# Performance work log

Hardware: AMD Instinct MI355X
Metric: run time of the kernel (lower is better)

Reference implementation:

```python
import jax, jax.numpy as jnp
import numpy as np

N_HEAD = 16
NEG = -1.0e9


def setup_inputs() -> dict:
    key = jax.random.key(0)
    k1, k2, k3 = jax.random.split(key, 3)
    B, T, C = 4, 2048, 1024
    x = jax.random.normal(k1, (B, T, C), dtype=jnp.float32)
    # torch Linear(C, 3C, bias=False): weight [3C, C], y = x @ W.T
    w_attn = jax.random.normal(k2, (3 * C, C), dtype=jnp.float32) * (1.0 / np.sqrt(C))
    w_proj = jax.random.normal(k3, (C, C), dtype=jnp.float32) * (1.0 / np.sqrt(C))
    return {"x": x, "w_attn": w_attn, "w_proj": w_proj}


def reference(x, w_attn, w_proj):
    B, T, C = x.shape
    hd = C // N_HEAD
    qkv = x @ w_attn.T  # [B,T,3C]
    q, k, v = jnp.split(qkv, 3, axis=2)
    # [B,T,C] -> [B,H,T,hd]
    q = q.reshape(B, T, N_HEAD, hd).transpose(0, 2, 1, 3)
    k = k.reshape(B, T, N_HEAD, hd).transpose(0, 2, 1, 3)
    v = v.reshape(B, T, N_HEAD, hd).transpose(0, 2, 1, 3)
    att = jnp.einsum('bhqd,bhkd->bhqk', q, k) * (1.0 / np.sqrt(hd))
    causal = jnp.tril(jnp.ones((T, T), dtype=bool))
    att = jnp.where(causal[None, None, :, :], att, NEG)
    att = jax.nn.softmax(att, axis=-1)
    y = jnp.einsum('bhqk,bhkd->bhqd', att, v)  # [B,H,T,hd]
    y = y.transpose(0, 2, 1, 3).reshape(B, T, C)
    return y @ w_proj.T
```

## Files before the change

### kernel.cpp

```cpp
#include <hip/hip_runtime.h>
#include <hip/hip_bf16.h>

typedef __bf16 bf16x8_t __attribute__((ext_vector_type(8)));
typedef __bf16 bf16x4_t __attribute__((ext_vector_type(4)));
typedef float f32x4_t __attribute__((ext_vector_type(4)));

__device__ __forceinline__ void gload_lds16(const void* g, void* l) {
    __builtin_amdgcn_global_load_lds((const __attribute__((address_space(1))) void*)g,
                                     (__attribute__((address_space(3))) void*)l, 16, 0, 0);
}

__global__ void f2bf_kernel(const float* __restrict__ in, __bf16* __restrict__ out, int n) {
    int i = (blockIdx.x * blockDim.x + threadIdx.x) * 4;
    if (i >= n) return;
    float4 v = *(const float4*)(in + i);
    bf16x4_t o;
    o[0] = (__bf16)v.x; o[1] = (__bf16)v.y; o[2] = (__bf16)v.z; o[3] = (__bf16)v.w;
    *(bf16x4_t*)(out + i) = o;
}

template <typename OutT>
__global__ __launch_bounds__(256) void gemm_bt(const __bf16* __restrict__ A,
                                               const __bf16* __restrict__ Bt,
                                               OutT* __restrict__ C,
                                               int M, int N, int K) {
    __shared__ __bf16 As[128 * 32];
    __shared__ __bf16 Bs[128 * 32];

    const int tid  = threadIdx.x;
    const int lane = tid & 63;
    const int wid  = tid >> 6;
    const int wm   = wid >> 1;
    const int wn   = wid & 1;

    const int nwg = gridDim.x * gridDim.y;
    int fl = blockIdx.y * gridDim.x + blockIdx.x;
    fl = (fl & 7) * (nwg >> 3) + (fl >> 3);
    const int m0 = (fl / gridDim.x) * 128;
    const int n0 = (fl % gridDim.x) * 128;

    const int lr = lane & 15;
    const int lk = (lane >> 4) * 8;
    const int cr = (lane >> 4) * 4;

    f32x4_t acc[4][4];
    for (int i = 0; i < 4; ++i)
        for (int j = 0; j < 4; ++j)
            acc[i][j] = (f32x4_t){0.f, 0.f, 0.f, 0.f};

    for (int k0 = 0; k0 < K; k0 += 32) {
        __syncthreads();
        for (int i = 0; i < 2; ++i) {
            int flat = i * 256 + tid;
            int row  = flat >> 2;
            int col  = (flat & 3) * 8;
            gload_lds16(&A[(size_t)(m0 + row) * K + k0 + col], &As[(size_t)(i * 256 + wid * 64) * 8]);
            gload_lds16(&Bt[(size_t)(n0 + row) * K + k0 + col], &Bs[(size_t)(i * 256 + wid * 64) * 8]);
        }
        __syncthreads();

        bf16x8_t af[4], bfr[4];
        for (int mf = 0; mf < 4; ++mf)
            af[mf] = *(const bf16x8_t*)&As[(wm * 64 + mf * 16 + lr) * 32 + lk];
        for (int nf = 0; nf < 4; ++nf)
            bfr[nf] = *(const bf16x8_t*)&Bs[(wn * 64 + nf * 16 + lr) * 32 + lk];
        for (int mf = 0; mf < 4; ++mf)
            for (int nf = 0; nf < 4; ++nf)
                acc[mf][nf] = __builtin_amdgcn_mfma_f32_16x16x32_bf16(af[mf], bfr[nf], acc[mf][nf], 0, 0, 0);
    }

    for (int mf = 0; mf < 4; ++mf)
        for (int nf = 0; nf < 4; ++nf)
            for (int r = 0; r < 4; ++r) {
                int row = m0 + wm * 64 + mf * 16 + cr + r;
                int col = n0 + wn * 64 + nf * 16 + lr;
                C[(size_t)row * N + col] = (OutT)acc[mf][nf][r];
            }
}

__global__ __launch_bounds__(512, 4) void attn_kernel(const __bf16* __restrict__ qkv,
                                                      __bf16* __restrict__ y) {
    const int T = 2048, C3 = 3072;
    const int orig = blockIdx.x;
    const int bidx = ((orig & 7) << 6) + (orig >> 3);
    const int pair = bidx & 7;
    const int h    = (bidx >> 3) & 15;
    const int b    = bidx >> 7;

    __shared__ __bf16 Ks[128 * 64];
    __shared__ __bf16 Vt[2][64 * 72];
    __shared__ __bf16 Ps[8 * 16 * 136];

    const int tid  = threadIdx.x;
    const int lane = tid & 63;
    const int w    = tid >> 6;
    const int lr   = lane & 15;
    const int lg   = lane >> 4;
    const int lk   = lg * 8;

    const __bf16* qg = qkv + (size_t)b * T * C3 + h * 64;
    const __bf16* kg = qg + 1024;
    const __bf16* vg = qg + 2048;

    const float CE    = 0.125f * 1.44269504f;
    const float DEFER = 44.0f;

    const int r0    = tid >> 3;
    const int kcol  = (tid & 7) * 8;
    const int kslot = ((tid & 7) ^ (r0 & 7)) << 3;
    const int vks   = r0 ^ ((tid & 7) << 3);

    __bf16* Pw = &Ps[w * 16 * 136];

    for (int pass = 0; pass < 2; ++pass) {
        const int qs  = pass ? 15 - pair : pair;
        const int qt0 = qs * 128;
        const int nt  = qs + 1;

        bf16x8_t qf0, qf1;
        {
            const __bf16* qrow = qg + (size_t)(qt0 + w * 16 + lr) * C3;
            qf0 = *(const bf16x8_t*)&qrow[lk];
            qf1 = *(const bf16x8_t*)&qrow[32 + lk];
        }

        bf16x8_t ka = *(const bf16x8_t*)&kg[(size_t)r0 * C3 + kcol];
        bf16x8_t kb = *(const bf16x8_t*)&kg[(size_t)(64 + r0) * C3 + kcol];
        bf16x8_t va = *(const bf16x8_t*)&vg[(size_t)r0 * C3 + kcol];
        bf16x8_t vb = *(const bf16x8_t*)&vg[(size_t)(64 + r0) * C3 + kcol];

        f32x4_t o_acc[4];
#pragma unroll
        for (int i = 0; i < 4; ++i) o_acc[i] = (f32x4_t){0.f, 0.f, 0.f, 0.f};
        float m_r = -3.0e38f, l_r = 0.f;

        for (int t = 0; t < nt; ++t) {
            __syncthreads();

            *(bf16x8_t*)&Ks[r0 * 64 + kslot] = ka;
            *(bf16x8_t*)&Ks[(64 + r0) * 64 + kslot] = kb;
#pragma unroll
            for (int j = 0; j < 8; ++j) Vt[0][(kcol + j) * 72 + vks] = va[j];
#pragma unroll
            for (int j = 0; j < 8; ++j) Vt[1][(kcol + j) * 72 + vks] = vb[j];

            __syncthreads();

            if (t + 1 < nt) {
                const size_t kb0 = (size_t)(t + 1) * 128;
                ka = *(const bf16x8_t*)&kg[(kb0 + r0) * C3 + kcol];
                kb = *(const bf16x8_t*)&kg[(kb0 + 64 + r0) * C3 + kcol];
                va = *(const bf16x8_t*)&vg[(kb0 + r0) * C3 + kcol];
                vb = *(const bf16x8_t*)&vg[(kb0 + 64 + r0) * C3 + kcol];
            }

            f32x4_t s[8];
#pragma unroll
            for (int c = 0; c < 8; ++c) {
                const int key = c * 16 + lr;
                const int sw  = (key & 7) << 3;
                bf16x8_t kfa = *(const bf16x8_t*)&Ks[key * 64 + (lk ^ sw)];
                bf16x8_t kfb = *(const bf16x8_t*)&Ks[key * 64 + ((32 + lk) ^ sw)];
                s[c] = __builtin_amdgcn_mfma_f32_16x16x32_bf16(kfa, qf0, (f32x4_t){0.f, 0.f, 0.f, 0.f}, 0, 0, 0);
                s[c] = __builtin_amdgcn_mfma_f32_16x16x32_bf16(kfb, qf1, s[c], 0, 0, 0);
            }

            if (t == nt - 1) {
                const int ql = w * 16 + lr;
#pragma unroll
                for (int c = 0; c < 8; ++c)
#pragma unroll
                    for (int r = 0; r < 4; ++r)
                        if (c * 16 + lg * 4 + r > ql) s[c][r] = -1.0e30f;
            }

            float pm = s[0][0];
#pragma unroll
            for (int c = 0; c < 8; ++c)
#pragma unroll
                for (int r = 0; r < 4; ++r) pm = fmaxf(pm, s[c][r]);

            if (!__all(pm <= m_r + DEFER)) {
                pm = fmaxf(pm, __shfl_xor(pm, 16));
                pm = fmaxf(pm, __shfl_xor(pm, 32));
                const float mn    = fmaxf(m_r, pm);
                const float alpha = exp2f((m_r - mn) * CE);
                l_r *= alpha;
#pragma unroll
                for (int dt = 0; dt < 4; ++dt)
#pragma unroll
                    for (int r = 0; r < 4; ++r) o_acc[dt][r] *= alpha;
                m_r = mn;
            }
            const float mce = m_r * CE;

            float rs = 0.f;
#pragma unroll
            for (int c = 0; c < 8; ++c) {
                bf16x4_t pk;
#pragma unroll
                for (int r = 0; r < 4; ++r) {
                    float pv = exp2f(fmaf(s[c][r], CE, -mce));
                    rs += pv;
                    pk[r] = (__bf16)pv;
                }
                *(bf16x4_t*)&Pw[lr * 136 + c * 16 + lg * 4] = pk;
            }
            rs += __shfl_xor(rs, 16);
            rs += __shfl_xor(rs, 32);
            l_r += rs;

#pragma unroll
            for (int hf = 0; hf < 2; ++hf) {
                bf16x8_t pb0 = *(const bf16x8_t*)&Pw[lr * 136 + hf * 64 + lk];
                bf16x8_t pb1 = *(const bf16x8_t*)&Pw[lr * 136 + hf * 64 + 32 + lk];
#pragma unroll
                for (int dt = 0; dt < 4; ++dt) {
                    const int d   = dt * 16 + lr;
                    const int sw2 = ((d >> 3) & 7) << 3;
                    bf16x8_t vb0 = *(const bf16x8_t*)&Vt[hf][d * 72 + (lk ^ sw2)];
                    bf16x8_t vb1 = *(const bf16x8_t*)&Vt[hf][d * 72 + ((32 + lk) ^ sw2)];
                    o_acc[dt] = __builtin_amdgcn_mfma_f32_16x16x32_bf16(vb0, pb0, o_acc[dt], 0, 0, 0);
                    o_acc[dt] = __builtin_amdgcn_mfma_f32_16x16x32_bf16(vb1, pb1, o_acc[dt], 0, 0, 0);
                }
            }
        }

        const float inv = 1.0f / l_r;
        const int q = qt0 + w * 16 + lr;
#pragma unroll
        for (int dt = 0; dt < 4; ++dt) {
            bf16x4_t ov;
#pragma unroll
            for (int r = 0; r < 4; ++r) ov[r] = (__bf16)(o_acc[dt][r] * inv);
            *(bf16x4_t*)&y[(size_t)(b * T + q) * 1024 + h * 64 + dt * 16 + lg * 4] = ov;
        }
    }
}

extern "C" void kernel_launch(void* const* d_in, const int* in_sizes, int n_in,
                              void* d_out, int out_size, void* d_ws, size_t ws_size,
                              hipStream_t stream) {
    const float* x      = (const float*)d_in[0];
    const float* w_attn = (const float*)d_in[1];
    const float* w_proj = (const float*)d_in[2];
    float* out = (float*)d_out;

    char* ws = (char*)d_ws;
    __bf16* xb   = (__bf16*)(ws);
    __bf16* wab  = (__bf16*)(ws + 16777216);
    __bf16* wpb  = (__bf16*)(ws + 23068672);
    __bf16* qkvb = (__bf16*)(ws + 25165824);
    __bf16* yb   = (__bf16*)(ws + 75497472);

    f2bf_kernel<<<8192, 256, 0, stream>>>(x, xb, 8388608);
    f2bf_kernel<<<3072, 256, 0, stream>>>(w_attn, wab, 3145728);
    f2bf_kernel<<<1024, 256, 0, stream>>>(w_proj, wpb, 1048576);

    gemm_bt<__bf16><<<dim3(24, 64), 256, 0, stream>>>(xb, wab, qkvb, 8192, 3072, 1024);

    attn_kernel<<<512, 512, 0, stream>>>(qkvb, yb);

    gemm_bt<float><<<dim3(8, 64), 256, 0, stream>>>(yb, wpb, out, 8192, 1024, 1024);
}
```

Before: 190.9 us.

## Add 512-thread 128x256 double-buffered QKV GEMM with swizzled LDS and setprio

Replaces the QKV projection GEMM with a new kernel that uses 512-thread blocks and 128x256 output tiles with a K-step of 64. Tiles are double-buffered in LDS through direct global-to-LDS loads, with an XOR swizzle to avoid bank conflicts. A vmcnt-based wait lets the next tile's loads overlap the current tile's MFMAs, and s_setprio raises wave priority during the math. The larger tile is meant to improve operand reuse and hide load latency. In exchange it uses more LDS and registers per block, and the grid drops to 768 blocks.

```diff
diff --git a/kernel.cpp b/kernel.cpp
--- a/kernel.cpp
+++ b/kernel.cpp
@@ -17,6 +17,122 @@
     bf16x4_t o;
     o[0] = (__bf16)v.x; o[1] = (__bf16)v.y; o[2] = (__bf16)v.z; o[3] = (__bf16)v.w;
     *(bf16x4_t*)(out + i) = o;
+}
+
+__global__ __launch_bounds__(512, 2) void gemm1_8ph(const __bf16* __restrict__ A,
+                                                    const __bf16* __restrict__ Bt,
+                                                    __bf16* __restrict__ C,
+                                                    int M, int N, int K) {
+    __shared__ __bf16 AsB[2][16 * 512];
+    __shared__ __bf16 BsB[2][32 * 512];
+
+    const int tid  = threadIdx.x;
+    const int lane = tid & 63;
+    const int wid  = tid >> 6;
+    const int wm   = wid >> 2;
+    const int wn   = wid & 3;
+
+    const int nwg   = gridDim.x;
+    const int ntile = N >> 8;
+    int fl = blockIdx.x;
+    fl = (fl & 7) * (nwg >> 3) + (fl >> 3);
+    const int m0 = (fl / ntile) * 128;
+    const int n0 = (fl % ntile) * 256;
+
+    const int lr = lane & 15;
+    const int lg = lane >> 4;
+    const int cr = lg * 4;
+    const int srow = lane >> 3;
+    const int gcol = (((lane & 7) ^ srow) << 3);
+
+    f32x4_t acc[4][4];
+#pragma unroll
+    for (int i = 0; i < 4; ++i)
+#pragma unroll
+        for (int j = 0; j < 4; ++j)
+            acc[i][j] = (f32x4_t){0.f, 0.f, 0.f, 0.f};
+
+    const int NT = K >> 6;
+
+    auto stage = [&](int kt, int buf) {
+        const __bf16* Ab = A + (size_t)m0 * K + kt * 64;
+        const __bf16* Bb = Bt + (size_t)n0 * K + kt * 64;
+        __bf16* Al = &AsB[buf][0];
+        __bf16* Bl = &BsB[buf][0];
+#pragma unroll
+        for (int j = 0; j < 6; ++j) {
+            int seg = wid * 6 + j;
+            if (seg < 16) {
+                gload_lds16(Ab + (size_t)(seg * 8 + srow) * K + gcol, Al + seg * 512);
+            } else {
+                int s2 = seg - 16;
+                gload_lds16(Bb + (size_t)(s2 * 8 + srow) * K + gcol, Bl + s2 * 512);
+            }
+        }
+    };
+
+    stage(0, 0);
+
+    for (int kt = 0; kt < NT; ++kt) {
+        const int cur = kt & 1;
+        const bool pf = (kt + 1 < NT);
+        if (pf) stage(kt + 1, cur ^ 1);
+
+        if (pf) asm volatile("s_waitcnt vmcnt(6)" ::: "memory");
+        else    asm volatile("s_waitcnt vmcnt(0)" ::: "memory");
+        __builtin_amdgcn_sched_barrier(0);
+        __builtin_amdgcn_s_barrier();
+        __builtin_amdgcn_sched_barrier(0);
+
+        const __bf16* Al = &AsB[cur][0];
+        const __bf16* Bl = &BsB[cur][0];
+
+        bf16x8_t af[4][2];
+#pragma unroll
+        for (int mf = 0; mf < 4; ++mf)
+#pragma unroll
+            for (int kk = 0; kk < 2; ++kk) {
+                const int row = wm * 64 + mf * 16 + lr;
+                const int g   = kk * 4 + lg;
+                af[mf][kk] = *(const bf16x8_t*)&Al[row * 64 + ((g ^ (row & 7)) << 3)];
+            }
+
+#pragma unroll
+        for (int p = 0; p < 2; ++p) {
+            bf16x8_t bfr[2][2];
+#pragma unroll
+            for (int nfp = 0; nfp < 2; ++nfp)
+#pragma unroll
+                for (int kk = 0; kk < 2; ++kk) {
+                    const int row = wn * 64 + (p * 2 + nfp) * 16 + lr;
+                    const int g   = kk * 4 + lg;
+                    bfr[nfp][kk] = *(const bf16x8_t*)&Bl[row * 64 + ((g ^ (row & 7)) << 3)];
+                }
+            __builtin_amdgcn_s_setprio(1);
+#pragma unroll
+            for (int mf = 0; mf < 4; ++mf)
+#pragma unroll
+                for (int nfp = 0; nfp < 2; ++nfp) {
+                    const int nf = p * 2 + nfp;
+                    acc[mf][nf] = __builtin_amdgcn_mfma_f32_16x16x32_bf16(af[mf][0], bfr[nfp][0], acc[mf][nf], 0, 0, 0);
+                    acc[mf][nf] = __builtin_amdgcn_mfma_f32_16x16x32_bf16(af[mf][1], bfr[nfp][1], acc[mf][nf], 0, 0, 0);
+                }
+            __builtin_amdgcn_s_setprio(0);
+            __builtin_amdgcn_s_barrier();
+        }
+        __builtin_amdgcn_sched_barrier(0);
+    }
+
+#pragma unroll
+    for (int mf = 0; mf < 4; ++mf)
+#pragma unroll
+        for (int nf = 0; nf < 4; ++nf)
+#pragma unroll
+            for (int r = 0; r < 4; ++r) {
+                int row = m0 + wm * 64 + mf * 16 + cr + r;
+                int col = n0 + wn * 64 + nf * 16 + lr;
+                C[(size_t)row * N + col] = (__bf16)acc[mf][nf][r];
+            }
 }
 
 template <typename OutT>
@@ -257,7 +373,7 @@
     f2bf_kernel<<<3072, 256, 0, stream>>>(w_attn, wab, 3145728);
     f2bf_kernel<<<1024, 256, 0, stream>>>(w_proj, wpb, 1048576);
 
-    gemm_bt<__bf16><<<dim3(24, 64), 256, 0, stream>>>(xb, wab, qkvb, 8192, 3072, 1024);
+    gemm1_8ph<<<768, 512, 0, stream>>>(xb, wab, qkvb, 8192, 3072, 1024);
 
     attn_kernel<<<512, 512, 0, stream>>>(qkvb, yb);
 
```

Result: no change. 188.6 us (-1.2%).

## Rewrite GEMMs with triple-buffered LDS pipeline, 128x256 tiles and swizzled loads

Applied to the files above, without the earlier changes.

Replaces the single-buffered 128x128 GEMM with a 512-thread 128x256-tile kernel. It triple-buffers K=64 slices in LDS with async global-to-LDS loads, uses explicit vmcnt waits and barriers, and XOR-swizzles the LDS layout to avoid bank conflicts. The B loads are split into two halves interleaved with the MFMA phases, and s_setprio raises wave priority around the MFMA blocks. The goal is to hide global load latency and cut sync overhead per K step. The cost is much higher LDS use (144KB per block) and fewer resident blocks per CU.

```diff
diff --git a/kernel.cpp b/kernel.cpp
--- a/kernel.cpp
+++ b/kernel.cpp
@@ -20,57 +20,132 @@
 }
 
 template <typename OutT>
-__global__ __launch_bounds__(256) void gemm_bt(const __bf16* __restrict__ A,
-                                               const __bf16* __restrict__ Bt,
-                                               OutT* __restrict__ C,
-                                               int M, int N, int K) {
-    __shared__ __bf16 As[128 * 32];
-    __shared__ __bf16 Bs[128 * 32];
+__global__ __launch_bounds__(512, 2) void gemm_dp(const __bf16* __restrict__ A,
+                                                  const __bf16* __restrict__ Bt,
+                                                  OutT* __restrict__ C,
+                                                  int M, int N, int K) {
+    __shared__ __bf16 As[3][128 * 64];
+    __shared__ __bf16 Bs[3][256 * 64];
 
     const int tid  = threadIdx.x;
     const int lane = tid & 63;
     const int wid  = tid >> 6;
-    const int wm   = wid >> 1;
-    const int wn   = wid & 1;
-
-    const int nwg = gridDim.x * gridDim.y;
-    int fl = blockIdx.y * gridDim.x + blockIdx.x;
+    const int wm   = wid >> 2;
+    const int wn   = wid & 3;
+
+    const int nwg   = gridDim.x;
+    const int ntile = N >> 8;
+    int fl = blockIdx.x;
     fl = (fl & 7) * (nwg >> 3) + (fl >> 3);
-    const int m0 = (fl / gridDim.x) * 128;
-    const int n0 = (fl % gridDim.x) * 128;
+    const int m0 = (fl / ntile) * 128;
+    const int n0 = (fl % ntile) * 256;
 
     const int lr = lane & 15;
-    const int lk = (lane >> 4) * 8;
-    const int cr = (lane >> 4) * 4;
+    const int lg = lane >> 4;
+    const int cr = lg * 4;
+    const int srow = lane >> 3;
+    const int gcol = (((lane & 7) ^ srow) << 3);
 
     f32x4_t acc[4][4];
+#pragma unroll
     for (int i = 0; i < 4; ++i)
+#pragma unroll
         for (int j = 0; j < 4; ++j)
             acc[i][j] = (f32x4_t){0.f, 0.f, 0.f, 0.f};
 
-    for (int k0 = 0; k0 < K; k0 += 32) {
-        __syncthreads();
-        for (int i = 0; i < 2; ++i) {
-            int flat = i * 256 + tid;
-            int row  = flat >> 2;
-            int col  = (flat & 3) * 8;
-            gload_lds16(&A[(size_t)(m0 + row) * K + k0 + col], &As[(size_t)(i * 256 + wid * 64) * 8]);
-            gload_lds16(&Bt[(size_t)(n0 + row) * K + k0 + col], &Bs[(size_t)(i * 256 + wid * 64) * 8]);
-        }
-        __syncthreads();
-
-        bf16x8_t af[4], bfr[4];
+    const int NT = K >> 6;
+
+    auto stageA_B0 = [&](int kt, int buf) {
+        const __bf16* Ab = A + (size_t)m0 * K + kt * 64;
+        const __bf16* Bb = Bt + (size_t)n0 * K + kt * 64;
+        __bf16* Al = &As[buf][0];
+        __bf16* Bl = &Bs[buf][0];
+        gload_lds16(Ab + (size_t)(wid * 8 + srow) * K + gcol,        Al + wid * 512);
+        gload_lds16(Ab + (size_t)((wid + 8) * 8 + srow) * K + gcol,  Al + (wid + 8) * 512);
+        gload_lds16(Bb + (size_t)(wid * 8 + srow) * K + gcol,        Bl + wid * 512);
+        gload_lds16(Bb + (size_t)((wid + 8) * 8 + srow) * K + gcol,  Bl + (wid + 8) * 512);
+    };
+    auto stageB1 = [&](int kt, int buf) {
+        const __bf16* Bb = Bt + (size_t)n0 * K + kt * 64;
+        __bf16* Bl = &Bs[buf][0];
+        gload_lds16(Bb + (size_t)((wid + 16) * 8 + srow) * K + gcol, Bl + (wid + 16) * 512);
+        gload_lds16(Bb + (size_t)((wid + 24) * 8 + srow) * K + gcol, Bl + (wid + 24) * 512);
+    };
+
+    stageA_B0(0, 0); stageB1(0, 0);
+    stageA_B0(1, 1); stageB1(1, 1);
+
+    for (int kt = 0; kt < NT; ++kt) {
+        const int cur = kt % 3;
+        const int b2  = (kt + 2) % 3;
+        const bool pf = (kt + 2 < NT);
+
+        if (kt + 1 < NT) asm volatile("s_waitcnt vmcnt(6)" ::: "memory");
+        else             asm volatile("s_waitcnt vmcnt(0)" ::: "memory");
+        __builtin_amdgcn_sched_barrier(0);
+        __builtin_amdgcn_s_barrier();
+        __builtin_amdgcn_sched_barrier(0);
+
+        const __bf16* Al = &As[cur][0];
+        const __bf16* Bl = &Bs[cur][0];
+
+        if (pf) stageA_B0(kt + 2, b2);
+
+        bf16x8_t af[4][2];
+#pragma unroll
         for (int mf = 0; mf < 4; ++mf)
-            af[mf] = *(const bf16x8_t*)&As[(wm * 64 + mf * 16 + lr) * 32 + lk];
+#pragma unroll
+            for (int kk = 0; kk < 2; ++kk) {
+                const int row = wm * 64 + mf * 16 + lr;
+                const int g   = kk * 4 + lg;
+                af[mf][kk] = *(const bf16x8_t*)&Al[row * 64 + ((g ^ (row & 7)) << 3)];
+            }
+        bf16x8_t bfr[2][2];
+#pragma unroll
+        for (int nf = 0; nf < 2; ++nf)
+#pragma unroll
+            for (int kk = 0; kk < 2; ++kk) {
+                const int row = wn * 64 + nf * 16 + lr;
+                const int g   = kk * 4 + lg;
+                bfr[nf][kk] = *(const bf16x8_t*)&Bl[row * 64 + ((g ^ (row & 7)) << 3)];
+            }
+        __builtin_amdgcn_s_setprio(1);
+#pragma unroll
+        for (int mf = 0; mf < 4; ++mf)
+#pragma unroll
+            for (int nf = 0; nf < 2; ++nf) {
+                acc[mf][nf] = __builtin_amdgcn_mfma_f32_16x16x32_bf16(af[mf][0], bfr[nf][0], acc[mf][nf], 0, 0, 0);
+                acc[mf][nf] = __builtin_amdgcn_mfma_f32_16x16x32_bf16(af[mf][1], bfr[nf][1], acc[mf][nf], 0, 0, 0);
+            }
+        __builtin_amdgcn_s_setprio(0);
+        __builtin_amdgcn_s_barrier();
+
+        if (pf) stageB1(kt + 2, b2);
+#pragma unroll
+        for (int nf = 0; nf < 2; ++nf)
+#pragma unroll
+            for (int kk = 0; kk < 2; ++kk) {
+                const int row = wn * 64 + (2 + nf) * 16 + lr;
+                const int g   = kk * 4 + lg;
+                bfr[nf][kk] = *(const bf16x8_t*)&Bl[row * 64 + ((g ^ (row & 7)) << 3)];
+            }
+        __builtin_amdgcn_s_setprio(1);
+#pragma unroll
+        for (int mf = 0; mf < 4; ++mf)
+#pragma unroll
+            for (int nf = 0; nf < 2; ++nf) {
+                acc[mf][2 + nf] = __builtin_amdgcn_mfma_f32_16x16x32_bf16(af[mf][0], bfr[nf][0], acc[mf][2 + nf], 0, 0, 0);
+                acc[mf][2 + nf] = __builtin_amdgcn_mfma_f32_16x16x32_bf16(af[mf][1], bfr[nf][1], acc[mf][2 + nf], 0, 0, 0);
+            }
+        __builtin_amdgcn_s_setprio(0);
+        __builtin_amdgcn_s_barrier();
+    }
+
+#pragma unroll
+    for (int mf = 0; mf < 4; ++mf)
+#pragma unroll
         for (int nf = 0; nf < 4; ++nf)
-            bfr[nf] = *(const bf16x8_t*)&Bs[(wn * 64 + nf * 16 + lr) * 32 + lk];
-        for (int mf = 0; mf < 4; ++mf)
-            for (int nf = 0; nf < 4; ++nf)
-                acc[mf][nf] = __builtin_amdgcn_mfma_f32_16x16x32_bf16(af[mf], bfr[nf], acc[mf][nf], 0, 0, 0);
-    }
-
-    for (int mf = 0; mf < 4; ++mf)
-        for (int nf = 0; nf < 4; ++nf)
+#pragma unroll
             for (int r = 0; r < 4; ++r) {
                 int row = m0 + wm * 64 + mf * 16 + cr + r;
                 int col = n0 + wn * 64 + nf * 16 + lr;
@@ -257,9 +332,9 @@
     f2bf_kernel<<<3072, 256, 0, stream>>>(w_attn, wab, 3145728);
     f2bf_kernel<<<1024, 256, 0, stream>>>(w_proj, wpb, 1048576);
 
-    gemm_bt<__bf16><<<dim3(24, 64), 256, 0, stream>>>(xb, wab, qkvb, 8192, 3072, 1024);
+    gemm_dp<__bf16><<<768, 512, 0, stream>>>(xb, wab, qkvb, 8192, 3072, 1024);
 
     attn_kernel<<<512, 512, 0, stream>>>(qkvb, yb);
 
-    gemm_bt<float><<<dim3(8, 64), 256, 0, stream>>>(yb, wpb, out, 8192, 1024, 1024);
-}
+    gemm_dp<float><<<256, 512, 0, stream>>>(yb, wpb, out, 8192, 1024, 1024);
+}
```

Result: slower. 206.5 us (+8.2%).

## Give each attention wave two 16-row query tiles, halving block threads

Applied to the files above, without the earlier changes.

The attention block drops from 8 waves of 16 query rows to 4 waves of 32 rows. Each wave now reuses the K fragments it loads from LDS across two query tiles, and the V fragments across two P tiles. This halves LDS fragment reads per MFMA, and each thread stages twice as much K/V data per tile. The cost is roughly twice the accumulator and score registers per thread, which may lower occupancy, plus fewer waves available to hide latency.

```diff
diff --git a/kernel.cpp b/kernel.cpp
--- a/kernel.cpp
+++ b/kernel.cpp
@@ -78,7 +78,7 @@
             }
 }
 
-__global__ __launch_bounds__(512, 4) void attn_kernel(const __bf16* __restrict__ qkv,
+__global__ __launch_bounds__(256, 2) void attn_kernel(const __bf16* __restrict__ qkv,
                                                       __bf16* __restrict__ y) {
     const int T = 2048, C3 = 3072;
     const int orig = blockIdx.x;
@@ -89,7 +89,7 @@
 
     __shared__ __bf16 Ks[128 * 64];
     __shared__ __bf16 Vt[2][64 * 72];
-    __shared__ __bf16 Ps[8 * 16 * 136];
+    __shared__ __bf16 Ps[4 * 32 * 136];
 
     const int tid  = threadIdx.x;
     const int lane = tid & 63;
@@ -105,135 +105,173 @@
     const float CE    = 0.125f * 1.44269504f;
     const float DEFER = 44.0f;
 
-    const int r0    = tid >> 3;
-    const int kcol  = (tid & 7) * 8;
-    const int kslot = ((tid & 7) ^ (r0 & 7)) << 3;
-    const int vks   = r0 ^ ((tid & 7) << 3);
-
-    __bf16* Pw = &Ps[w * 16 * 136];
+    const int kr  = tid >> 1;
+    const int kc0 = (tid & 1) * 4;
+    const int vr  = tid >> 2;
+    const int vc0 = (tid & 3) * 2;
+
+    __bf16* Pw = &Ps[w * 32 * 136];
 
     for (int pass = 0; pass < 2; ++pass) {
         const int qs  = pass ? 15 - pair : pair;
         const int qt0 = qs * 128;
         const int nt  = qs + 1;
 
-        bf16x8_t qf0, qf1;
-        {
-            const __bf16* qrow = qg + (size_t)(qt0 + w * 16 + lr) * C3;
-            qf0 = *(const bf16x8_t*)&qrow[lk];
-            qf1 = *(const bf16x8_t*)&qrow[32 + lk];
+        bf16x8_t qa[2], qb[2];
+#pragma unroll
+        for (int qf = 0; qf < 2; ++qf) {
+            const __bf16* qrow = qg + (size_t)(qt0 + w * 32 + qf * 16 + lr) * C3;
+            qa[qf] = *(const bf16x8_t*)&qrow[lk];
+            qb[qf] = *(const bf16x8_t*)&qrow[32 + lk];
         }
 
-        bf16x8_t ka = *(const bf16x8_t*)&kg[(size_t)r0 * C3 + kcol];
-        bf16x8_t kb = *(const bf16x8_t*)&kg[(size_t)(64 + r0) * C3 + kcol];
-        bf16x8_t va = *(const bf16x8_t*)&vg[(size_t)r0 * C3 + kcol];
-        bf16x8_t vb = *(const bf16x8_t*)&vg[(size_t)(64 + r0) * C3 + kcol];
-
-        f32x4_t o_acc[4];
-#pragma unroll
-        for (int i = 0; i < 4; ++i) o_acc[i] = (f32x4_t){0.f, 0.f, 0.f, 0.f};
-        float m_r = -3.0e38f, l_r = 0.f;
+        bf16x8_t kv[4], vv[4];
+#pragma unroll
+        for (int j = 0; j < 4; ++j)
+            kv[j] = *(const bf16x8_t*)&kg[(size_t)kr * C3 + (kc0 + j) * 8];
+#pragma unroll
+        for (int hf = 0; hf < 2; ++hf)
+#pragma unroll
+            for (int u = 0; u < 2; ++u)
+                vv[hf * 2 + u] = *(const bf16x8_t*)&vg[(size_t)(hf * 64 + vr) * C3 + (vc0 + u) * 8];
+
+        f32x4_t o_acc[2][4];
+#pragma unroll
+        for (int qf = 0; qf < 2; ++qf)
+#pragma unroll
+            for (int i = 0; i < 4; ++i) o_acc[qf][i] = (f32x4_t){0.f, 0.f, 0.f, 0.f};
+        float m_r[2] = {-3.0e38f, -3.0e38f};
+        float l_r[2] = {0.f, 0.f};
 
         for (int t = 0; t < nt; ++t) {
             __syncthreads();
 
-            *(bf16x8_t*)&Ks[r0 * 64 + kslot] = ka;
-            *(bf16x8_t*)&Ks[(64 + r0) * 64 + kslot] = kb;
-#pragma unroll
-            for (int j = 0; j < 8; ++j) Vt[0][(kcol + j) * 72 + vks] = va[j];
-#pragma unroll
-            for (int j = 0; j < 8; ++j) Vt[1][(kcol + j) * 72 + vks] = vb[j];
+#pragma unroll
+            for (int j = 0; j < 4; ++j)
+                *(bf16x8_t*)&Ks[kr * 64 + (((kc0 + j) ^ (kr & 7)) << 3)] = kv[j];
+#pragma unroll
+            for (int hf = 0; hf < 2; ++hf)
+#pragma unroll
+                for (int u = 0; u < 2; ++u) {
+                    const int c  = vc0 + u;
+                    const int ks = vr ^ (c << 3);
+#pragma unroll
+                    for (int j = 0; j < 8; ++j)
+                        Vt[hf][(c * 8 + j) * 72 + ks] = vv[hf * 2 + u][j];
+                }
 
             __syncthreads();
 
             if (t + 1 < nt) {
                 const size_t kb0 = (size_t)(t + 1) * 128;
-                ka = *(const bf16x8_t*)&kg[(kb0 + r0) * C3 + kcol];
-                kb = *(const bf16x8_t*)&kg[(kb0 + 64 + r0) * C3 + kcol];
-                va = *(const bf16x8_t*)&vg[(kb0 + r0) * C3 + kcol];
-                vb = *(const bf16x8_t*)&vg[(kb0 + 64 + r0) * C3 + kcol];
-            }
-
-            f32x4_t s[8];
+#pragma unroll
+                for (int j = 0; j < 4; ++j)
+                    kv[j] = *(const bf16x8_t*)&kg[(kb0 + kr) * C3 + (kc0 + j) * 8];
+#pragma unroll
+                for (int hf = 0; hf < 2; ++hf)
+#pragma unroll
+                    for (int u = 0; u < 2; ++u)
+                        vv[hf * 2 + u] = *(const bf16x8_t*)&vg[(kb0 + hf * 64 + vr) * C3 + (vc0 + u) * 8];
+            }
+
+            f32x4_t s0[8], s1[8];
 #pragma unroll
             for (int c = 0; c < 8; ++c) {
                 const int key = c * 16 + lr;
                 const int sw  = (key & 7) << 3;
                 bf16x8_t kfa = *(const bf16x8_t*)&Ks[key * 64 + (lk ^ sw)];
                 bf16x8_t kfb = *(const bf16x8_t*)&Ks[key * 64 + ((32 + lk) ^ sw)];
-                s[c] = __builtin_amdgcn_mfma_f32_16x16x32_bf16(kfa, qf0, (f32x4_t){0.f, 0.f, 0.f, 0.f}, 0, 0, 0);
-                s[c] = __builtin_amdgcn_mfma_f32_16x16x32_bf16(kfb, qf1, s[c], 0, 0, 0);
+                s0[c] = __builtin_amdgcn_mfma_f32_16x16x32_bf16(kfa, qa[0], (f32x4_t){0.f, 0.f, 0.f, 0.f}, 0, 0, 0);
+                s0[c] = __builtin_amdgcn_mfma_f32_16x16x32_bf16(kfb, qb[0], s0[c], 0, 0, 0);
+                s1[c] = __builtin_amdgcn_mfma_f32_16x16x32_bf16(kfa, qa[1], (f32x4_t){0.f, 0.f, 0.f, 0.f}, 0, 0, 0);
+                s1[c] = __builtin_amdgcn_mfma_f32_16x16x32_bf16(kfb, qb[1], s1[c], 0, 0, 0);
             }
 
             if (t == nt - 1) {
-                const int ql = w * 16 + lr;
 #pragma unroll
                 for (int c = 0; c < 8; ++c)
 #pragma unroll
-                    for (int r = 0; r < 4; ++r)
-                        if (c * 16 + lg * 4 + r > ql) s[c][r] = -1.0e30f;
-            }
-
-            float pm = s[0][0];
-#pragma unroll
-            for (int c = 0; c < 8; ++c)
-#pragma unroll
-                for (int r = 0; r < 4; ++r) pm = fmaxf(pm, s[c][r]);
-
-            if (!__all(pm <= m_r + DEFER)) {
-                pm = fmaxf(pm, __shfl_xor(pm, 16));
-                pm = fmaxf(pm, __shfl_xor(pm, 32));
-                const float mn    = fmaxf(m_r, pm);
-                const float alpha = exp2f((m_r - mn) * CE);
-                l_r *= alpha;
-#pragma unroll
-                for (int dt = 0; dt < 4; ++dt)
-#pragma unroll
-                    for (int r = 0; r < 4; ++r) o_acc[dt][r] *= alpha;
-                m_r = mn;
-            }
-            const float mce = m_r * CE;
-
-            float rs = 0.f;
-#pragma unroll
-            for (int c = 0; c < 8; ++c) {
-                bf16x4_t pk;
-#pragma unroll
-                for (int r = 0; r < 4; ++r) {
-                    float pv = exp2f(fmaf(s[c][r], CE, -mce));
-                    rs += pv;
-                    pk[r] = (__bf16)pv;
-                }
-                *(bf16x4_t*)&Pw[lr * 136 + c * 16 + lg * 4] = pk;
-            }
-            rs += __shfl_xor(rs, 16);
-            rs += __shfl_xor(rs, 32);
-            l_r += rs;
+                    for (int r = 0; r < 4; ++r) {
+                        const int ko = c * 16 + lg * 4 + r;
+                        if (ko > w * 32 + lr)      s0[c][r] = -1.0e30f;
+                        if (ko > w * 32 + 16 + lr) s1[c][r] = -1.0e30f;
+                    }
+            }
+
+#pragma unroll
+            for (int qf = 0; qf < 2; ++qf) {
+                f32x4_t* s = qf ? s1 : s0;
+                float pm = s[0][0];
+#pragma unroll
+                for (int c = 0; c < 8; ++c)
+#pragma unroll
+                    for (int r = 0; r < 4; ++r) pm = fmaxf(pm, s[c][r]);
+
+                if (!__all(pm <= m_r[qf] + DEFER)) {
+                    pm = fmaxf(pm, __shfl_xor(pm, 16));
+                    pm = fmaxf(pm, __shfl_xor(pm, 32));
+                    const float mn    = fmaxf(m_r[qf], pm);
+                    const float alpha = exp2f((m_r[qf] - mn) * CE);
+                    l_r[qf] *= alpha;
+#pragma unroll
+                    for (int dt = 0; dt < 4; ++dt)
+#pragma unroll
+                        for (int r = 0; r < 4; ++r) o_acc[qf][dt][r] *= alpha;
+                    m_r[qf] = mn;
+                }
+                const float mce = m_r[qf] * CE;
+
+                float rs = 0.f;
+#pragma unroll
+                for (int c = 0; c < 8; ++c) {
+                    bf16x4_t pk;
+#pragma unroll
+                    for (int r = 0; r < 4; ++r) {
+                        float pv = exp2f(fmaf(s[c][r], CE, -mce));
+                        rs += pv;
+                        pk[r] = (__bf16)pv;
+                    }
+                    *(bf16x4_t*)&Pw[(qf * 16 + lr) * 136 + c * 16 + lg * 4] = pk;
+                }
+                rs += __shfl_xor(rs, 16);
+                rs += __shfl_xor(rs, 32);
+                l_r[qf] += rs;
+            }
 
 #pragma unroll
             for (int hf = 0; hf < 2; ++hf) {
-                bf16x8_t pb0 = *(const bf16x8_t*)&Pw[lr * 136 + hf * 64 + lk];
-                bf16x8_t pb1 = *(const bf16x8_t*)&Pw[lr * 136 + hf * 64 + 32 + lk];
+                bf16x8_t pb0[2], pb1[2];
+#pragma unroll
+                for (int qf = 0; qf < 2; ++qf) {
+                    pb0[qf] = *(const bf16x8_t*)&Pw[(qf * 16 + lr) * 136 + hf * 64 + lk];
+                    pb1[qf] = *(const bf16x8_t*)&Pw[(qf * 16 + lr) * 136 + hf * 64 + 32 + lk];
+                }
 #pragma unroll
                 for (int dt = 0; dt < 4; ++dt) {
                     const int d   = dt * 16 + lr;
                     const int sw2 = ((d >> 3) & 7) << 3;
                     bf16x8_t vb0 = *(const bf16x8_t*)&Vt[hf][d * 72 + (lk ^ sw2)];
                     bf16x8_t vb1 = *(const bf16x8_t*)&Vt[hf][d * 72 + ((32 + lk) ^ sw2)];
-                    o_acc[dt] = __builtin_amdgcn_mfma_f32_16x16x32_bf16(vb0, pb0, o_acc[dt], 0, 0, 0);
-                    o_acc[dt] = __builtin_amdgcn_mfma_f32_16x16x32_bf16(vb1, pb1, o_acc[dt], 0, 0, 0);
+#pragma unroll
+                    for (int qf = 0; qf < 2; ++qf) {
+                        o_acc[qf][dt] = __builtin_amdgcn_mfma_f32_16x16x32_bf16(vb0, pb0[qf], o_acc[qf][dt], 0, 0, 0);
+                        o_acc[qf][dt] = __builtin_amdgcn_mfma_f32_16x16x32_bf16(vb1, pb1[qf], o_acc[qf][dt], 0, 0, 0);
+                    }
                 }
             }
         }
 
-        const float inv = 1.0f / l_r;
-        const int q = qt0 + w * 16 + lr;
-#pragma unroll
-        for (int dt = 0; dt < 4; ++dt) {
-            bf16x4_t ov;
-#pragma unroll
-            for (int r = 0; r < 4; ++r) ov[r] = (__bf16)(o_acc[dt][r] * inv);
-            *(bf16x4_t*)&y[(size_t)(b * T + q) * 1024 + h * 64 + dt * 16 + lg * 4] = ov;
+#pragma unroll
+        for (int qf = 0; qf < 2; ++qf) {
+            const float inv = 1.0f / l_r[qf];
+            const int q = qt0 + w * 32 + qf * 16 + lr;
+#pragma unroll
+            for (int dt = 0; dt < 4; ++dt) {
+                bf16x4_t ov;
+#pragma unroll
+                for (int r = 0; r < 4; ++r) ov[r] = (__bf16)(o_acc[qf][dt][r] * inv);
+                *(bf16x4_t*)&y[(size_t)(b * T + q) * 1024 + h * 64 + dt * 16 + lg * 4] = ov;
+            }
         }
     }
 }
@@ -259,7 +297,7 @@
 
     gemm_bt<__bf16><<<dim3(24, 64), 256, 0, stream>>>(xb, wab, qkvb, 8192, 3072, 1024);
 
-    attn_kernel<<<512, 512, 0, stream>>>(qkvb, yb);
+    attn_kernel<<<512, 256, 0, stream>>>(qkvb, yb);
 
     gemm_bt<float><<<dim3(8, 64), 256, 0, stream>>>(yb, wpb, out, 8192, 1024, 1024);
 }
```

New measurement: 199.1 us. 1.04x slower.
